# Performance work log

Measured on AMD Instinct MI355X. Metric: run time of the kernel, lower is better.

Reference implementation:

```python
import jax, jax.numpy as jnp
import numpy as np

N_NODES = 100000
N_EDGES_DIR = 400000
IN_CH = 200
OUT_CH = 200
NUM_REL = 237
NUM_BASIS = 50


def setup_inputs() -> dict:
    key = jax.random.key(0)
    ks = jax.random.split(key, 10)
    inv_sqrt = 1.0 / np.sqrt(IN_CH)
    return {
        "nodes_features": jax.random.normal(ks[0], (N_NODES, IN_CH), dtype=jnp.float32),
        "edge_index": jax.random.randint(ks[1], (2, 2 * N_EDGES_DIR), 0, N_NODES, dtype=jnp.int64),
        "edge_type": jax.random.randint(ks[2], (2 * N_EDGES_DIR,), 0, 2 * NUM_REL, dtype=jnp.int64),
        "basis_vector": jax.random.uniform(ks[3], (NUM_BASIS, IN_CH), dtype=jnp.float32, minval=-inv_sqrt, maxval=inv_sqrt),
        "rel_weight": jax.random.uniform(ks[4], (2 * NUM_REL, NUM_BASIS), dtype=jnp.float32, minval=-0.1, maxval=0.1),
        "weight_rel": jax.random.uniform(ks[5], (IN_CH, OUT_CH), dtype=jnp.float32, minval=-inv_sqrt, maxval=inv_sqrt),
        "loop_rel": jax.random.uniform(ks[6], (1, IN_CH), dtype=jnp.float32, minval=-inv_sqrt, maxval=inv_sqrt),
        "w_in": jax.random.uniform(ks[7], (IN_CH, OUT_CH), dtype=jnp.float32, minval=-inv_sqrt, maxval=inv_sqrt),
        "w_out": jax.random.uniform(ks[8], (IN_CH, OUT_CH), dtype=jnp.float32, minval=-inv_sqrt, maxval=inv_sqrt),
        "w_loop": jax.random.uniform(ks[9], (IN_CH, OUT_CH), dtype=jnp.float32, minval=-inv_sqrt, maxval=inv_sqrt),
    }


def _edge_norm(head, tail, num_nodes):
    # symmetric GCN norm: deg^{-1/2}[head] * deg^{-1/2}[tail] (inf -> 0)
    ones = jnp.ones(head.shape[0], dtype=jnp.float32)
    deg = jax.ops.segment_sum(ones, head, num_segments=num_nodes)
    dinv = jnp.where(deg > 0, jax.lax.rsqrt(jnp.maximum(deg, 1e-30)), 0.0)
    return dinv[head] * dinv[tail]


def _propagate(x, rel_emb, ei, et, norm, W, num_nodes):
    # gather -> compose(sub) -> matmul -> scale -> scatter(sum)
    msg = x[ei[1]] - rel_emb[et]          # [E, in]
    out = msg @ W                          # [E, out]
    if norm is not None:
        out = out * norm[:, None]
    return jax.ops.segment_sum(out, ei[0], num_segments=num_nodes)


def reference(nodes_features, edge_index, edge_type, basis_vector, rel_weight,
              weight_rel, loop_rel, w_in, w_out, w_loop):
    num_nodes = nodes_features.shape[0]
    rel_emb = jnp.concatenate([rel_weight @ basis_vector, loop_rel], axis=0)  # [2R+1, in]
    half = edge_index.shape[1] // 2
    in_idx, out_idx = edge_index[:, :half], edge_index[:, half:]
    in_t, out_t = edge_type[:half], edge_type[half:]
    in_norm = _edge_norm(in_idx[0], in_idx[1], num_nodes)
    out_norm = _edge_norm(out_idx[0], out_idx[1], num_nodes)
    in_res = _propagate(nodes_features, rel_emb, in_idx, in_t, in_norm, w_in, num_nodes)
    out_res = _propagate(nodes_features, rel_emb, out_idx, out_t, out_norm, w_out, num_nodes)
    # loop pass: loop_index is identity, loop relation is the last rel_emb row (= loop_rel)
    loop_res = (nodes_features - loop_rel) @ w_loop
    out = jnp.tanh((in_res + out_res + loop_res) * (1.0 / 3.0))  # dropout = identity (eval)
    out_2 = rel_emb @ weight_rel
    return out, out_2
```

## Files before the change

kernel.cpp:

```cpp
#include <hip/hip_runtime.h>

#define NN 100000
#define NE 400000
#define NE2 800000
#define C 200
#define NREL 475
#define NB 50
#define NSCAN_BLKS ((2 * NN + 255) / 256)

#define NWTB  ((3 * 16 * 7 * 64 + 255) / 256)
#define NXLB  ((NN * 100 + 255) / 256)
#define NDEGB ((NE2 + 255) / 256)
#define G_WT    (NREL)
#define G_XLOOP (G_WT + NWTB)
#define G_DEG   (G_XLOOP + NXLB)
#define NPREB   (G_DEG + NDEGB)

typedef __attribute__((ext_vector_type(8))) short short8;
typedef __attribute__((ext_vector_type(4))) float f32x4;
typedef __attribute__((ext_vector_type(2))) float f32x2;
typedef __attribute__((ext_vector_type(2))) unsigned u32x2;
typedef __attribute__((ext_vector_type(4))) unsigned u32x4;

#define W_RE     0L
#define W_DINV   95104L
#define W_DEG    295104L
#define W_OFFS   495104L
#define W_PSUM   695200L
#define W_BUCKET 696320L
#define W_BNORM  1496320L
#define W_AGG    2296320L
#define W_WT     32309120L
#define W_REB    32395264L

__device__ __forceinline__ unsigned short f2bf(float f) {
  unsigned u = __builtin_bit_cast(unsigned, f);
  return (unsigned short)((u + 0x7FFFu + ((u >> 16) & 1u)) >> 16);
}
__device__ __forceinline__ unsigned pack2(float a, float b) {
  return (unsigned)f2bf(a) | ((unsigned)f2bf(b) << 16);
}
__device__ __forceinline__ float bf_lo(unsigned w) { return __builtin_bit_cast(float, w << 16); }
__device__ __forceinline__ float bf_hi(unsigned w) { return __builtin_bit_cast(float, w & 0xFFFF0000u); }


__global__ void k_pre(const float* rw, const float* basis, const float* loop_rel,
                      const float* wrel, float* re, float* out2, unsigned* reb,
                      const float* w_in, const float* w_out, const float* w_loop,
                      short* wtsw, const float* x, unsigned* agg2,
                      const int* ei, int* deg) {
  int b = blockIdx.x;
  int j = threadIdx.x;
  if (b < G_WT) {
    __shared__ float srow[C];
    __shared__ float brow[NB];
    int r = b;
    if (j < NB && r < NREL - 1) brow[j] = rw[r * NB + j];
    __syncthreads();
    if (j < C) {
      float v;
      if (r == NREL - 1) {
        v = loop_rel[j];
      } else {
        v = 0.f;
        #pragma unroll 5
        for (int bb = 0; bb < NB; bb++) v += brow[bb] * basis[bb * C + j];
      }
      srow[j] = v;
      re[(size_t)r * C + j] = v;
    }
    __syncthreads();
    if (j < C) {
      float a = 0.f;
      #pragma unroll 4
      for (int k = 0; k < C; k++) a += srow[k] * wrel[k * C + j];
      out2[(size_t)r * C + j] = a;
    }
    if (j < 100) {
      int ch = 2 * j;
      reb[(size_t)r * 100 + j] = pack2(srow[ch] - loop_rel[ch], srow[ch + 1] - loop_rel[ch + 1]);
    }
  } else if (b < G_XLOOP) {
    int i = (b - G_WT) * 256 + j;
    if (i >= 3 * 16 * 7 * 64) return;
    int l = i & 63;
    int rest = i >> 6;
    int ks = rest % 7;
    int rest2 = rest / 7;
    int ct = rest2 & 15;
    int mat = rest2 >> 4;
    const float* W = (mat == 0) ? w_in : (mat == 1) ? w_out : w_loop;
    int n = ct * 16 + (l & 15);
    int kb = ks * 32 + (l >> 4) * 8;
    short8 v;
    #pragma unroll
    for (int q = 0; q < 8; q++) {
      int k = kb + q;
      v[q] = (n < C && k < C) ? (short)f2bf(W[k * C + n]) : (short)0;
    }
    *(short8*)(wtsw + (size_t)i * 8) = v;
  } else if (b < G_DEG) {
    int i = (b - G_XLOOP) * 256 + j;
    if (i >= NN * 100) return;
    int n = i / 100, w = i - n * 100;
    int ch = 2 * w;
    f32x2 v = *(const f32x2*)(x + (size_t)n * C + ch);
    f32x2 l = *(const f32x2*)(loop_rel + ch);
    agg2[i] = pack2(v[0] - l[0], v[1] - l[1]);
  } else {
    int c = (b - G_DEG) * 256 + j;
    if (c >= NE2) return;
    atomicAdd(deg + (c < NE ? 0 : NN) + ei[c], 1);
  }
}


__global__ void k_scan1(const int* deg, int* psum, float* dinv) {
  __shared__ int s[256];
  int t = threadIdx.x, i = blockIdx.x * 256 + t;
  int v = (i < 2 * NN) ? deg[i] : 0;
  if (i < 2 * NN) dinv[i] = (v > 0) ? rsqrtf((float)v) : 0.f;
  s[t] = v;
  __syncthreads();
  for (int off = 128; off > 0; off >>= 1) {
    if (t < off) s[t] += s[t + off];
    __syncthreads();
  }
  if (t == 0) psum[blockIdx.x] = s[0];
}

__global__ void k_scan2(int* psum) {
  __shared__ int s[1024];
  int t = threadIdx.x;
  int v = (t < NSCAN_BLKS) ? psum[t] : 0;
  s[t] = v;
  __syncthreads();
  for (int off = 1; off < 1024; off <<= 1) {
    int x = (t >= off) ? s[t - off] : 0;
    __syncthreads();
    s[t] += x;
    __syncthreads();
  }
  if (t < NSCAN_BLKS) psum[t] = s[t] - v;
}

__global__ void k_scan3(const int* deg, const int* psum, int* offs, int* cursor) {
  __shared__ int s[256];
  int t = threadIdx.x, i = blockIdx.x * 256 + t;
  int v = (i < 2 * NN) ? deg[i] : 0;
  s[t] = v;
  __syncthreads();
  for (int off = 1; off < 256; off <<= 1) {
    int x = (t >= off) ? s[t - off] : 0;
    __syncthreads();
    s[t] += x;
    __syncthreads();
  }
  if (i < 2 * NN) {
    int o = psum[blockIdx.x] + s[t] - v;
    offs[i] = o;
    cursor[i] = o;
  }
  if (i == 0) offs[2 * NN] = NE2;
}

__global__ void k_scatter(const int* ei, const int* et, const float* dinv,
                          int* cursor, unsigned* bucket, float* bnorm) {
  int c = blockIdx.x * blockDim.x + threadIdx.x;
  if (c >= NE2) return;
  int head = ei[c];
  int tail = ei[NE2 + c];
  int ty = et[c];
  int base = (c < NE) ? 0 : NN;
  float nm = dinv[base + head] * dinv[base + tail];
  int pos = atomicAdd(cursor + base + head, 1);
  bucket[pos] = ((unsigned)tail << 9) | (unsigned)ty;
  bnorm[pos] = nm;
}


__global__ __launch_bounds__(256) void k_gather(const unsigned* __restrict__ bucket,
                                                const int* __restrict__ offs,
                                                const float* __restrict__ bnorm,
                                                const unsigned* __restrict__ xb,
                                                const unsigned* __restrict__ reb,
                                                unsigned* __restrict__ agg) {
  int wid = (blockIdx.x * blockDim.x + threadIdx.x) >> 6;
  if (wid >= 2 * NN) return;
  int lane = threadIdx.x & 63;
  int s = offs[wid], e = offs[wid + 1];
  bool act = lane < 50;
  int wo = 2 * lane;
  float a0 = 0.f, a1 = 0.f, a2 = 0.f, a3 = 0.f;
  int p = s;
  for (; p + 3 < e; p += 4) {
    unsigned w0 = bucket[p],     w1 = bucket[p + 1];
    unsigned w2 = bucket[p + 2], w3 = bucket[p + 3];
    float n0 = bnorm[p],     n1 = bnorm[p + 1];
    float n2 = bnorm[p + 2], n3 = bnorm[p + 3];
    int t0 = (int)(w0 >> 9), y0 = (int)(w0 & 511u);
    int t1 = (int)(w1 >> 9), y1 = (int)(w1 & 511u);
    int t2 = (int)(w2 >> 9), y2 = (int)(w2 & 511u);
    int t3 = (int)(w3 >> 9), y3 = (int)(w3 & 511u);
    if (act) {
      u32x2 xv0 = *(const u32x2*)(xb + (size_t)t0 * 100 + wo);
      u32x2 rv0 = *(const u32x2*)(reb + (size_t)y0 * 100 + wo);
      u32x2 xv1 = *(const u32x2*)(xb + (size_t)t1 * 100 + wo);
      u32x2 rv1 = *(const u32x2*)(reb + (size_t)y1 * 100 + wo);
      u32x2 xv2 = *(const u32x2*)(xb + (size_t)t2 * 100 + wo);
      u32x2 rv2 = *(const u32x2*)(reb + (size_t)y2 * 100 + wo);
      u32x2 xv3 = *(const u32x2*)(xb + (size_t)t3 * 100 + wo);
      u32x2 rv3 = *(const u32x2*)(reb + (size_t)y3 * 100 + wo);
      a0 += n0 * (bf_lo(xv0[0]) - bf_lo(rv0[0]));
      a1 += n0 * (bf_hi(xv0[0]) - bf_hi(rv0[0]));
      a2 += n0 * (bf_lo(xv0[1]) - bf_lo(rv0[1]));
      a3 += n0 * (bf_hi(xv0[1]) - bf_hi(rv0[1]));
      a0 += n1 * (bf_lo(xv1[0]) - bf_lo(rv1[0]));
      a1 += n1 * (bf_hi(xv1[0]) - bf_hi(rv1[0]));
      a2 += n1 * (bf_lo(xv1[1]) - bf_lo(rv1[1]));
      a3 += n1 * (bf_hi(xv1[1]) - bf_hi(rv1[1]));
      a0 += n2 * (bf_lo(xv2[0]) - bf_lo(rv2[0]));
      a1 += n2 * (bf_hi(xv2[0]) - bf_hi(rv2[0]));
      a2 += n2 * (bf_lo(xv2[1]) - bf_lo(rv2[1]));
      a3 += n2 * (bf_hi(xv2[1]) - bf_hi(rv2[1]));
      a0 += n3 * (bf_lo(xv3[0]) - bf_lo(rv3[0]));
      a1 += n3 * (bf_hi(xv3[0]) - bf_hi(rv3[0]));
      a2 += n3 * (bf_lo(xv3[1]) - bf_lo(rv3[1]));
      a3 += n3 * (bf_hi(xv3[1]) - bf_hi(rv3[1]));
    }
  }
  for (; p < e; ++p) {
    unsigned w0 = bucket[p];
    float n0 = bnorm[p];
    int t0 = (int)(w0 >> 9), y0 = (int)(w0 & 511u);
    if (act) {
      u32x2 xv0 = *(const u32x2*)(xb + (size_t)t0 * 100 + wo);
      u32x2 rv0 = *(const u32x2*)(reb + (size_t)y0 * 100 + wo);
      a0 += n0 * (bf_lo(xv0[0]) - bf_lo(rv0[0]));
      a1 += n0 * (bf_hi(xv0[0]) - bf_hi(rv0[0]));
      a2 += n0 * (bf_lo(xv0[1]) - bf_lo(rv0[1]));
      a3 += n0 * (bf_hi(xv0[1]) - bf_hi(rv0[1]));
    }
  }
  if (act) {
    u32x2 o;
    o[0] = pack2(a0, a1);
    o[1] = pack2(a2, a3);
    *(u32x2*)(agg + (size_t)wid * 100 + wo) = o;
  }
}


__global__ __launch_bounds__(256, 4) void k_mm(const unsigned* __restrict__ agg,
                                               const short* __restrict__ wt,
                                               float* __restrict__ out) {
  __shared__ __align__(16) unsigned la[6464];
  int tid = threadIdx.x;
  int wave = tid >> 6;
  int lane = tid & 63;
  int m = lane & 15, kq = lane >> 4;
  int row0 = blockIdx.x * 64;
  int cw = (wave + blockIdx.x) & 3;

  f32x4 acc[4][4];
  #pragma unroll
  for (int s = 0; s < 4; s++)
    #pragma unroll
    for (int t = 0; t < 4; t++) acc[s][t] = (f32x4)(0.f);

  for (int mat = 0; mat < 3; mat++) {
    __syncthreads();
    const u32x4* src = (const u32x4*)(agg + ((size_t)mat * NN + row0) * 100);
    for (int idx = tid; idx < 1600; idx += 256)
      ((u32x4*)la)[idx] = src[idx];
    if (tid < 64) la[6400 + tid] = 0;
    __syncthreads();

    #pragma unroll
    for (int ks = 0; ks < 7; ks++) {
      short8 A[4], B[4];
      #pragma unroll
      for (int s = 0; s < 4; s++)
        A[s] = *(const short8*)(la + (size_t)(s * 16 + m) * 100 + kq * 4 + ks * 16);
      #pragma unroll
      for (int t = 0; t < 4; t++) {
        int g = cw * 4 + t;
        if (g < 13)
          B[t] = *(const short8*)(wt + ((size_t)((mat * 16 + g) * 7 + ks) * 64 + lane) * 8);
      }
      #pragma unroll
      for (int s = 0; s < 4; s++)
        #pragma unroll
        for (int t = 0; t < 4; t++)
          if (cw * 4 + t < 13)
            acc[s][t] = __builtin_amdgcn_mfma_f32_16x16x32_bf16(A[s], B[t], acc[s][t], 0, 0, 0);
    }
  }

  #pragma unroll
  for (int s = 0; s < 4; s++) {
    int r0 = row0 + s * 16 + kq * 4;
    #pragma unroll
    for (int t = 0; t < 4; t++) {
      int n = cw * 64 + t * 16 + m;
      if (n >= C) continue;
      #pragma unroll
      for (int j = 0; j < 4; j++) {
        int r = r0 + j;
        if (r < NN)
          __builtin_nontemporal_store(tanhf(acc[s][t][j] * (1.f / 3.f)),
                                      &out[(size_t)r * C + n]);
      }
    }
  }
}


extern "C" void kernel_launch(void* const* d_in, const int* in_sizes, int n_in,
                              void* d_out, int out_size, void* d_ws, size_t ws_size,
                              hipStream_t stream) {
  const float* X        = (const float*)d_in[0];
  const int*   ei       = (const int*)d_in[1];
  const int*   et       = (const int*)d_in[2];
  const float* basis    = (const float*)d_in[3];
  const float* relw     = (const float*)d_in[4];
  const float* wrel     = (const float*)d_in[5];
  const float* loop_rel = (const float*)d_in[6];
  const float* w_in     = (const float*)d_in[7];
  const float* w_out    = (const float*)d_in[8];
  const float* w_loop   = (const float*)d_in[9];

  float* out = (float*)d_out;
  float* ws  = (float*)d_ws;

  float*    re     = ws + W_RE;
  float*    dinv   = ws + W_DINV;
  int*      deg    = (int*)(ws + W_DEG);
  int*      offs   = (int*)(ws + W_OFFS);
  int*      psum   = (int*)(ws + W_PSUM);
  unsigned* bucket = (unsigned*)(ws + W_BUCKET);
  float*    bnorm  = ws + W_BNORM;
  unsigned* agg    = (unsigned*)(ws + W_AGG);
  short*    wt     = (short*)(ws + W_WT);
  unsigned* reb    = (unsigned*)(ws + W_REB);
  float*    out2   = out + (size_t)NN * C;
  unsigned* agg2   = agg + (size_t)2 * NN * 100;

  hipMemsetAsync(deg, 0, 2 * NN * sizeof(int), stream);

  k_pre<<<NPREB, 256, 0, stream>>>(relw, basis, loop_rel, wrel, re, out2, reb,
                                   w_in, w_out, w_loop, wt, X, agg2, ei, deg);

  k_scan1<<<NSCAN_BLKS, 256, 0, stream>>>(deg, psum, dinv);
  k_scan2<<<1, 1024, 0, stream>>>(psum);
  k_scan3<<<NSCAN_BLKS, 256, 0, stream>>>(deg, psum, offs, deg );
  k_scatter<<<(NE2 + 255) / 256, 256, 0, stream>>>(ei, et, dinv, deg , bucket, bnorm);

  k_gather<<<(2 * NN) / 4, 256, 0, stream>>>(bucket, offs, bnorm, agg2, reb, agg);
  k_mm<<<(NN + 63) / 64, 256, 0, stream>>>(agg, wt, out);
}
```

Measured before the change: 295.2 us.

## Store aggregates in MFMA fragment layout so matmul reads A directly

The gather and pre kernels now write the bf16 aggregated features in a per-16-row tile, per-k-step layout that matches the MFMA A-operand lane order. The matmul kernel can then load A fragments straight from global memory and no longer stages them through LDS, which removes two barriers per matrix and the shared-memory traffic. In exchange, x is converted to bf16 twice (a row-major copy for the gather and a fragment-layout copy for the loop term), and the gather writes become scattered 8-byte stores.

```diff
diff --git a/kernel.cpp b/kernel.cpp
--- a/kernel.cpp
+++ b/kernel.cpp
@@ -6,14 +6,17 @@
 #define C 200
 #define NREL 475
 #define NB 50
+#define NTILES 6250
 #define NSCAN_BLKS ((2 * NN + 255) / 256)
 
 #define NWTB  ((3 * 16 * 7 * 64 + 255) / 256)
+#define NXFB  ((NTILES * 7 * 128) / 256)
 #define NXLB  ((NN * 100 + 255) / 256)
 #define NDEGB ((NE2 + 255) / 256)
 #define G_WT    (NREL)
-#define G_XLOOP (G_WT + NWTB)
-#define G_DEG   (G_XLOOP + NXLB)
+#define G_XF    (G_WT + NWTB)
+#define G_XL    (G_XF + NXFB)
+#define G_DEG   (G_XL + NXLB)
 #define NPREB   (G_DEG + NDEGB)
 
 typedef __attribute__((ext_vector_type(8))) short short8;
@@ -29,9 +32,10 @@
 #define W_PSUM   695200L
 #define W_BUCKET 696320L
 #define W_BNORM  1496320L
-#define W_AGG    2296320L
-#define W_WT     32309120L
-#define W_REB    32395264L
+#define W_XB     2296320L
+#define W_AGGF   12296320L
+#define W_WT     45899904L
+#define W_REB    45985920L
 
 __device__ __forceinline__ unsigned short f2bf(float f) {
   unsigned u = __builtin_bit_cast(unsigned, f);
@@ -47,7 +51,7 @@
 __global__ void k_pre(const float* rw, const float* basis, const float* loop_rel,
                       const float* wrel, float* re, float* out2, unsigned* reb,
                       const float* w_in, const float* w_out, const float* w_loop,
-                      short* wtsw, const float* x, unsigned* agg2,
+                      short* wtsw, const float* x, unsigned* aggF, unsigned* xb,
                       const int* ei, int* deg) {
   int b = blockIdx.x;
   int j = threadIdx.x;
@@ -80,7 +84,7 @@
       int ch = 2 * j;
       reb[(size_t)r * 100 + j] = pack2(srow[ch] - loop_rel[ch], srow[ch + 1] - loop_rel[ch + 1]);
     }
-  } else if (b < G_XLOOP) {
+  } else if (b < G_XF) {
     int i = (b - G_WT) * 256 + j;
     if (i >= 3 * 16 * 7 * 64) return;
     int l = i & 63;
@@ -99,14 +103,33 @@
       v[q] = (n < C && k < C) ? (short)f2bf(W[k * C + n]) : (short)0;
     }
     *(short8*)(wtsw + (size_t)i * 8) = v;
+  } else if (b < G_XL) {
+    int i = (b - G_XF) * 256 + j;
+    int pr = i & 1;
+    int lane = (i >> 1) & 63;
+    int ks = (i >> 7) % 7;
+    int tile = i / 896;
+    int kq = lane >> 4, m = lane & 15;
+    int node = tile * 16 + m;
+    int w0 = ks * 16 + kq * 4 + 2 * pr;
+    u32x2 o;
+    if (w0 < 100) {
+      f32x4 v = *(const f32x4*)(x + (size_t)node * C + 2 * w0);
+      f32x4 l = *(const f32x4*)(loop_rel + 2 * w0);
+      o[0] = pack2(v[0] - l[0], v[1] - l[1]);
+      o[1] = pack2(v[2] - l[2], v[3] - l[3]);
+    } else {
+      o[0] = 0u; o[1] = 0u;
+    }
+    *(u32x2*)(aggF + ((size_t)(2 * NTILES + tile) * 7 + ks) * 256 + lane * 4 + 2 * pr) = o;
   } else if (b < G_DEG) {
-    int i = (b - G_XLOOP) * 256 + j;
+    int i = (b - G_XL) * 256 + j;
     if (i >= NN * 100) return;
     int n = i / 100, w = i - n * 100;
     int ch = 2 * w;
     f32x2 v = *(const f32x2*)(x + (size_t)n * C + ch);
     f32x2 l = *(const f32x2*)(loop_rel + ch);
-    agg2[i] = pack2(v[0] - l[0], v[1] - l[1]);
+    xb[i] = pack2(v[0] - l[0], v[1] - l[1]);
   } else {
     int c = (b - G_DEG) * 256 + j;
     if (c >= NE2) return;
@@ -184,7 +207,7 @@
                                                 const float* __restrict__ bnorm,
                                                 const unsigned* __restrict__ xb,
                                                 const unsigned* __restrict__ reb,
-                                                unsigned* __restrict__ agg) {
+                                                unsigned* __restrict__ aggF) {
   int wid = (blockIdx.x * blockDim.x + threadIdx.x) >> 6;
   if (wid >= 2 * NN) return;
   int lane = threadIdx.x & 63;
@@ -246,15 +269,19 @@
     u32x2 o;
     o[0] = pack2(a0, a1);
     o[1] = pack2(a2, a3);
-    *(u32x2*)(agg + (size_t)wid * 100 + wo) = o;
-  }
-}
-
-
-__global__ __launch_bounds__(256, 4) void k_mm(const unsigned* __restrict__ agg,
+    int mat = (wid >= NN) ? 1 : 0;
+    int node = wid - mat * NN;
+    int ks = wo >> 4;
+    int rr = wo & 15;
+    size_t f = ((size_t)mat * NTILES + (node >> 4)) * 7 + ks;
+    *(u32x2*)(aggF + f * 256 + (size_t)((rr >> 2) * 16 + (node & 15)) * 4 + (rr & 3)) = o;
+  }
+}
+
+
+__global__ __launch_bounds__(256, 4) void k_mm(const unsigned* __restrict__ aggF,
                                                const short* __restrict__ wt,
                                                float* __restrict__ out) {
-  __shared__ __align__(16) unsigned la[6464];
   int tid = threadIdx.x;
   int wave = tid >> 6;
   int lane = tid & 63;
@@ -269,19 +296,13 @@
     for (int t = 0; t < 4; t++) acc[s][t] = (f32x4)(0.f);
 
   for (int mat = 0; mat < 3; mat++) {
-    __syncthreads();
-    const u32x4* src = (const u32x4*)(agg + ((size_t)mat * NN + row0) * 100);
-    for (int idx = tid; idx < 1600; idx += 256)
-      ((u32x4*)la)[idx] = src[idx];
-    if (tid < 64) la[6400 + tid] = 0;
-    __syncthreads();
-
+    size_t tbase = (size_t)mat * NTILES + (row0 >> 4);
     #pragma unroll
     for (int ks = 0; ks < 7; ks++) {
       short8 A[4], B[4];
       #pragma unroll
       for (int s = 0; s < 4; s++)
-        A[s] = *(const short8*)(la + (size_t)(s * 16 + m) * 100 + kq * 4 + ks * 16);
+        A[s] = *(const short8*)(aggF + ((tbase + s) * 7 + ks) * 256 + lane * 4);
       #pragma unroll
       for (int t = 0; t < 4; t++) {
         int g = cw * 4 + t;
@@ -340,22 +361,22 @@
   int*      psum   = (int*)(ws + W_PSUM);
   unsigned* bucket = (unsigned*)(ws + W_BUCKET);
   float*    bnorm  = ws + W_BNORM;
-  unsigned* agg    = (unsigned*)(ws + W_AGG);
+  unsigned* xb     = (unsigned*)(ws + W_XB);
+  unsigned* aggF   = (unsigned*)(ws + W_AGGF);
   short*    wt     = (short*)(ws + W_WT);
   unsigned* reb    = (unsigned*)(ws + W_REB);
   float*    out2   = out + (size_t)NN * C;
-  unsigned* agg2   = agg + (size_t)2 * NN * 100;
 
   hipMemsetAsync(deg, 0, 2 * NN * sizeof(int), stream);
 
   k_pre<<<NPREB, 256, 0, stream>>>(relw, basis, loop_rel, wrel, re, out2, reb,
-                                   w_in, w_out, w_loop, wt, X, agg2, ei, deg);
+                                   w_in, w_out, w_loop, wt, X, aggF, xb, ei, deg);
 
   k_scan1<<<NSCAN_BLKS, 256, 0, stream>>>(deg, psum, dinv);
   k_scan2<<<1, 1024, 0, stream>>>(psum);
   k_scan3<<<NSCAN_BLKS, 256, 0, stream>>>(deg, psum, offs, deg );
   k_scatter<<<(NE2 + 255) / 256, 256, 0, stream>>>(ei, et, dinv, deg , bucket, bnorm);
 
-  k_gather<<<(2 * NN) / 4, 256, 0, stream>>>(bucket, offs, bnorm, agg2, reb, agg);
-  k_mm<<<(NN + 63) / 64, 256, 0, stream>>>(agg, wt, out);
-}
+  k_gather<<<(2 * NN) / 4, 256, 0, stream>>>(bucket, offs, bnorm, xb, reb, aggF);
+  k_mm<<<(NN + 63) / 64, 256, 0, stream>>>(aggF, wt, out);
+}
```

After: 363.3 us. 23.1% more time.
